# Kernel tuning notes

Measured on AMD Instinct MI355X. Metric: run time of the kernel, lower is better.

## Reference

```python
import jax, jax.numpy as jnp
import numpy as np

K = 3  # neighbors per sampled point (SetFeatureAbstraction k=3)


def fps_single(points, n_samples):
    """Farthest point sampling over one frame. points: [N, D]. Returns [n_samples] int32 idxs.
    Faithful to the torch loop: start at index 0, maintain min-distance-to-selected,
    pick argmax among remaining (selected points are masked to -inf)."""
    n = points.shape[0]

    def step(carry, _):
        dist, last = carry
        d = jnp.sum((points - points[last]) ** 2, axis=-1)   # squared dist to last added
        dist = jnp.minimum(dist, d)
        sel = jnp.argmax(dist).astype(jnp.int32)
        dist = dist.at[sel].set(-jnp.inf)                    # exclude from remaining
        return (dist, sel), sel

    dist0 = jnp.full((n,), jnp.inf, points.dtype).at[0].set(-jnp.inf)
    _, idxs = jax.lax.scan(step, (dist0, jnp.int32(0)), None, length=n_samples - 1)
    return jnp.concatenate([jnp.zeros((1,), jnp.int32), idxs])


def setup_inputs() -> dict:
    key = jax.random.key(0)
    ks = jax.random.split(key, 20)
    B, N, F, A, SD = 4, 8192, 64, 64, 5
    scale = lambda fan_in: 1.0 / np.sqrt(fan_in)
    def lin(k1, k2, out_d, in_d):
        s = scale(in_d)
        return (jax.random.uniform(k1, (out_d, in_d), jnp.float32, -s, s),
                jax.random.uniform(k2, (out_d,), jnp.float32, -s, s))
    w_in, b_in = lin(ks[0], ks[1], A, F)
    w_q, b_q = lin(ks[2], ks[3], A, A)
    w_k, b_k = lin(ks[4], ks[5], A, A)
    w_v, b_v = lin(ks[6], ks[7], A, A)
    w_h1, b_h1 = lin(ks[8], ks[9], A, A)
    w_h2, b_h2 = lin(ks[10], ks[11], A, A)
    w_out, b_out = lin(ks[12], ks[13], F, A)
    x = jax.random.normal(ks[14], (B, N, F), jnp.float32)
    spatial = jax.random.normal(ks[15], (B, N, SD), jnp.float32)
    return {"x": x, "spatial": spatial,
            "w_in": w_in, "b_in": b_in, "w_q": w_q, "b_q": b_q,
            "w_k": w_k, "b_k": b_k, "w_v": w_v, "b_v": b_v,
            "w_h1": w_h1, "b_h1": b_h1, "w_h2": w_h2, "b_h2": b_h2,
            "w_out": w_out, "b_out": b_out}


def reference(x, spatial, w_in, b_in, w_q, b_q, w_k, b_k, w_v, b_v,
              w_h1, b_h1, w_h2, b_h2, w_out, b_out):
    B, N, F = x.shape
    S = N // 2
    # ---- farthest point sampling (vmapped over batch) ----
    sample_idxs = jax.vmap(lambda p: fps_single(p, S))(spatial)          # [B, S]
    xs = jnp.take_along_axis(x, sample_idxs[..., None], axis=1)          # [B, S, F]
    sp = jnp.take_along_axis(spatial, sample_idxs[..., None], axis=1)    # [B, S, 5]
    # ---- kNN grouping: each sampled point gathers K nearest neighbors from full cloud ----
    d = jnp.sum((sp[:, :, None, :] - spatial[:, None, :, :]) ** 2, -1)   # [B, S, N]
    bidx = jnp.arange(B)[:, None]
    sidx = jnp.arange(S)[None, :]
    d = d.at[bidx, sidx, sample_idxs].set(jnp.inf)                        # exclude self
    _, knn_idx = jax.lax.top_k(-d, K)                                     # [B, S, K] smallest dists
    neigh_feat = jax.vmap(lambda xf, idx: xf[idx])(x, knn_idx)            # [B, S, K, F]
    # ---- subtract-based vector attention on sampled features ----
    t = xs @ w_in.T + b_in                                                # [B, S, A]
    q = t @ w_q.T + b_q
    k = t @ w_k.T + b_k
    v = t @ w_v.T + b_v
    h = jax.nn.relu((q - k) @ w_h1.T + b_h1) @ w_h2.T + b_h2
    w = jax.nn.softmax(h, axis=-1)                                        # per-channel weights
    out = (w * v) @ w_out.T + b_out + xs                                  # residual
    return out, neigh_feat
```

## Files before the change

kernel.cpp:

```cpp
#include <hip/hip_runtime.h>
#include <hip/hip_bf16.h>

#define NPTS 8192
#define SDIM 5
#define NBATCH 4
#define NS 4096
#define FEAT 64
#define KNN 3

#define WS_SIDX_OFF   0
#define WS_KNN_OFF    65536
#define WS_WT_OFF     262144

typedef float v2f __attribute__((ext_vector_type(2)));


__device__ __forceinline__ float sqdist5(float p0, float p1, float p2, float p3, float p4,
                                         float q0, float q1, float q2, float q3, float q4)
{
#pragma clang fp contract(off)
    float d0 = p0 - q0, d1 = p1 - q1, d2 = p2 - q2, d3 = p3 - q3, d4 = p4 - q4;
    float a = d0 * d0 + d1 * d1;
    a = a + d2 * d2;
    a = a + d3 * d3;
    a = a + d4 * d4;
    return a;
}

__device__ __forceinline__ float wave_max_f32_bcast(float v)
{
    int x;
    x = __builtin_amdgcn_update_dpp(0xFF800000, __float_as_int(v), 0x111, 0xf, 0xf, false);
    v = fmaxf(v, __int_as_float(x));
    x = __builtin_amdgcn_update_dpp(0xFF800000, __float_as_int(v), 0x112, 0xf, 0xf, false);
    v = fmaxf(v, __int_as_float(x));
    x = __builtin_amdgcn_update_dpp(0xFF800000, __float_as_int(v), 0x114, 0xf, 0xf, false);
    v = fmaxf(v, __int_as_float(x));
    x = __builtin_amdgcn_update_dpp(0xFF800000, __float_as_int(v), 0x118, 0xf, 0xf, false);
    v = fmaxf(v, __int_as_float(x));
    x = __builtin_amdgcn_update_dpp(0xFF800000, __float_as_int(v), 0x142, 0xf, 0xf, false);
    v = fmaxf(v, __int_as_float(x));
    x = __builtin_amdgcn_update_dpp(0xFF800000, __float_as_int(v), 0x143, 0xf, 0xf, false);
    v = fmaxf(v, __int_as_float(x));
    return __int_as_float(__builtin_amdgcn_readlane(__float_as_int(v), 63));
}

__device__ __forceinline__ int wave_min_i32_bcast(int v)
{
    int x;
    x = __builtin_amdgcn_update_dpp(0x7FFFFFFF, v, 0x111, 0xf, 0xf, false);
    v = min(v, x);
    x = __builtin_amdgcn_update_dpp(0x7FFFFFFF, v, 0x112, 0xf, 0xf, false);
    v = min(v, x);
    x = __builtin_amdgcn_update_dpp(0x7FFFFFFF, v, 0x114, 0xf, 0xf, false);
    v = min(v, x);
    x = __builtin_amdgcn_update_dpp(0x7FFFFFFF, v, 0x118, 0xf, 0xf, false);
    v = min(v, x);
    x = __builtin_amdgcn_update_dpp(0x7FFFFFFF, v, 0x142, 0xf, 0xf, false);
    v = min(v, x);
    x = __builtin_amdgcn_update_dpp(0x7FFFFFFF, v, 0x143, 0xf, 0xf, false);
    v = min(v, x);
    return __builtin_amdgcn_readlane(v, 63);
}

#define FOR_PAIRS(M) M(0) M(1) M(2) M(3) M(4) M(5) M(6) M(7)

__global__ __launch_bounds__(512, 2)
void fps_kernel(const float* __restrict__ spatial, int* __restrict__ sidx)
{
#pragma clang fp contract(off)
    const int b = blockIdx.x;
    const int t = threadIdx.x;
    const int lane = t & 63;
    const float* pts = spatial + (size_t)b * NPTS * SDIM;
    const float NEG_INF = -__builtin_inff();

#define DECL_PAIR(J) v2f px0_##J, px1_##J, px2_##J, px3_##J, px4_##J, dd_##J;
    FOR_PAIRS(DECL_PAIR)

#define LOAD_PAIR(J)                                                          \
    {                                                                         \
        const int ilo = (2 * J) * 512 + t;                                    \
        const int ihi = (2 * J + 1) * 512 + t;                                \
        px0_##J = (v2f){pts[ilo * SDIM + 0], pts[ihi * SDIM + 0]};            \
        px1_##J = (v2f){pts[ilo * SDIM + 1], pts[ihi * SDIM + 1]};            \
        px2_##J = (v2f){pts[ilo * SDIM + 2], pts[ihi * SDIM + 2]};            \
        px3_##J = (v2f){pts[ilo * SDIM + 3], pts[ihi * SDIM + 3]};            \
        px4_##J = (v2f){pts[ilo * SDIM + 4], pts[ihi * SDIM + 4]};            \
        dd_##J  = (v2f){__builtin_inff(), __builtin_inff()};                  \
    }
    FOR_PAIRS(LOAD_PAIR)

    if (t == 0) {
        dd_0.x = NEG_INF;
        sidx[b * NS] = 0;
    }

    __shared__ unsigned long long slot[4];
    if (t == 0) { slot[0] = 0; slot[1] = 0; slot[2] = 0; slot[3] = 0; }
    __syncthreads();

    int bsel = 0;
    for (int step = 1; step < NS; ++step) {
        const int p = step & 3;
        if (t == 0) slot[(step + 2) & 3] = 0;

        const float* qp = pts + bsel * SDIM;
        const float q0 = qp[0], q1 = qp[1], q2 = qp[2], q3 = qp[3], q4 = qp[4];
        const v2f q0v = {q0, q0}, q1v = {q1, q1}, q2v = {q2, q2},
                  q3v = {q3, q3}, q4v = {q4, q4};

        float bestv = NEG_INF;
        int   besti = 0;

#define UPD_PAIR(J)                                                           \
    {                                                                         \
        v2f t0 = px0_##J - q0v;                                               \
        v2f t1 = px1_##J - q1v;                                               \
        v2f t2 = px2_##J - q2v;                                               \
        v2f t3 = px3_##J - q3v;                                               \
        v2f t4 = px4_##J - q4v;                                               \
        v2f a = t0 * t0 + t1 * t1;      \
        a = a + t2 * t2;                                                      \
        a = a + t3 * t3;                                                      \
        a = a + t4 * t4;                                                      \
        v2f nd;                                                               \
        nd.x = fminf(dd_##J.x, a.x);                                          \
        nd.y = fminf(dd_##J.y, a.y);                                          \
        dd_##J = nd;                                                          \
        if (nd.x > bestv) { bestv = nd.x; besti = (2 * J) * 512 + t; }        \
        if (nd.y > bestv) { bestv = nd.y; besti = (2 * J + 1) * 512 + t; }    \
    }
        FOR_PAIRS(UPD_PAIR)

        const float maxv = wave_max_f32_bcast(bestv);
        const int   cand = (bestv == maxv) ? besti : 0x7FFFFFFF;
        const int   mini = wave_min_i32_bcast(cand);

        if (lane == 0) {
            const unsigned int kv = (maxv < 0.0f) ? 0u
                                                  : (__float_as_uint(maxv) | 0x80000000u);
            const unsigned long long key =
                ((unsigned long long)kv << 32) |
                (unsigned long long)(0xFFFFFFFFu - (unsigned)mini);
            atomicMax(&slot[p], key);
        }
        __syncthreads();

        const unsigned long long kk = slot[p];
        const int sel = (int)(0xFFFFFFFFu - (unsigned int)(kk & 0xFFFFFFFFull));
        bsel = __builtin_amdgcn_readfirstlane(sel);
        if (t == 0) sidx[b * NS + step] = sel;

        const int  jj  = bsel >> 9;
        const bool own = (bsel & 511) == t;

#define ZAP_PAIR(J)                                                           \
    {                                                                         \
        if (own && jj == 2 * J)     dd_##J.x = NEG_INF;                       \
        if (own && jj == 2 * J + 1) dd_##J.y = NEG_INF;                       \
    }
        FOR_PAIRS(ZAP_PAIR)
    }
}

__global__ __launch_bounds__(256)
void knn_kernel(const float* __restrict__ spatial, const int* __restrict__ sidx,
                int* __restrict__ knn)
{
    const int t   = threadIdx.x;
    const int sl  = t >> 3;
    const int r   = t & 7;
    const int spb = NS / 32;
    const int b   = blockIdx.x / spb;
    const int s   = (blockIdx.x % spb) * 32 + sl;
    const int self = sidx[b * NS + s];
    const float* pts = spatial + (size_t)b * NPTS * SDIM;

    const float q0 = pts[self * SDIM + 0], q1 = pts[self * SDIM + 1],
                q2 = pts[self * SDIM + 2], q3 = pts[self * SDIM + 3],
                q4 = pts[self * SDIM + 4];

    unsigned long long k0 = ~0ull, k1 = ~0ull, k2 = ~0ull;
    for (int i = r; i < NPTS; i += 8) {
        float a = sqdist5(pts[i * SDIM + 0], pts[i * SDIM + 1], pts[i * SDIM + 2],
                          pts[i * SDIM + 3], pts[i * SDIM + 4],
                          q0, q1, q2, q3, q4);
        unsigned long long key = ((unsigned long long)__float_as_uint(a) << 32) |
                                 (unsigned long long)(unsigned)i;
        if (i == self) key = ~0ull;
        if (key < k2) {
            if (key < k1) {
                k2 = k1;
                if (key < k0) { k1 = k0; k0 = key; } else k1 = key;
            } else k2 = key;
        }
    }

    __shared__ unsigned long long sk[256][3];
    sk[t][0] = k0; sk[t][1] = k1; sk[t][2] = k2;
    __syncthreads();

    if (r == 0) {
        unsigned long long b0 = ~0ull, b1 = ~0ull, b2 = ~0ull;
        for (int rr = 0; rr < 8; ++rr) {
#pragma unroll
            for (int m = 0; m < 3; ++m) {
                unsigned long long key = sk[(sl << 3) | rr][m];
                if (key < b2) {
                    if (key < b1) {
                        b2 = b1;
                        if (key < b0) { b1 = b0; b0 = key; } else b1 = key;
                    } else b2 = key;
                }
            }
        }
        const int basei = (b * NS + s) * KNN;
        knn[basei + 0] = (int)(b0 & 0xFFFFFFFFull);
        knn[basei + 1] = (int)(b1 & 0xFFFFFFFFull);
        knn[basei + 2] = (int)(b2 & 0xFFFFFFFFull);
    }
}

__global__ __launch_bounds__(256)
void gather_kernel(const float* __restrict__ x, const int* __restrict__ knn,
                   float* __restrict__ out2)
{
    const long long tid = (long long)blockIdx.x * 256 + threadIdx.x;
    const int       f   = (int)(tid & 63);
    const long long row = tid >> 6;
    const int       idx = knn[row];
    const int       b   = (int)(row / (NS * KNN));
    out2[tid] = x[((size_t)b * NPTS + idx) * FEAT + f];
}

__global__ __launch_bounds__(256)
void transpose_w(const float* __restrict__ w0, const float* __restrict__ w1,
                 const float* __restrict__ w2, const float* __restrict__ w3,
                 const float* __restrict__ w4, const float* __restrict__ w5,
                 const float* __restrict__ w6, float* __restrict__ wt)
{
    const float* w;
    switch (blockIdx.x) {
        case 0: w = w0; break; case 1: w = w1; break; case 2: w = w2; break;
        case 3: w = w3; break; case 4: w = w4; break; case 5: w = w5; break;
        default: w = w6; break;
    }
    float* o = wt + blockIdx.x * 4096;
    for (int e = threadIdx.x; e < 4096; e += 256) {
        const int r = e >> 6, c = e & 63;
        o[c * 64 + r] = w[e];
    }
}

__global__ __launch_bounds__(256)
void attn_kernel(const float* __restrict__ x, const int* __restrict__ sidx,
                 const float* __restrict__ wt,
                 const float* __restrict__ b_in, const float* __restrict__ b_q,
                 const float* __restrict__ b_k, const float* __restrict__ b_v,
                 const float* __restrict__ b_h1, const float* __restrict__ b_h2,
                 const float* __restrict__ b_out,
                 float* __restrict__ out)
{
    const int lane = threadIdx.x & 63;
    const int wid  = (int)((blockIdx.x * 256 + threadIdx.x) >> 6);
    const int b    = wid >> 12;
    const int si   = sidx[wid];
    const float xs = x[((size_t)b * NPTS + si) * FEAT + lane];

    const float* wt_in  = wt;
    const float* wt_q   = wt + 4096;
    const float* wt_k   = wt + 2 * 4096;
    const float* wt_v   = wt + 3 * 4096;
    const float* wt_h1  = wt + 4 * 4096;
    const float* wt_h2  = wt + 5 * 4096;
    const float* wt_out = wt + 6 * 4096;

    float tv = b_in[lane];
#pragma unroll
    for (int i = 0; i < 64; ++i) tv = fmaf(wt_in[i * 64 + lane], __shfl(xs, i), tv);

    float q = b_q[lane], k = b_k[lane], v = b_v[lane];
#pragma unroll
    for (int i = 0; i < 64; ++i) {
        const float ti = __shfl(tv, i);
        q = fmaf(wt_q[i * 64 + lane], ti, q);
        k = fmaf(wt_k[i * 64 + lane], ti, k);
        v = fmaf(wt_v[i * 64 + lane], ti, v);
    }
    const float d = q - k;
    float h = b_h1[lane];
#pragma unroll
    for (int i = 0; i < 64; ++i) h = fmaf(wt_h1[i * 64 + lane], __shfl(d, i), h);
    h = fmaxf(h, 0.0f);
    float h2 = b_h2[lane];
#pragma unroll
    for (int i = 0; i < 64; ++i) h2 = fmaf(wt_h2[i * 64 + lane], __shfl(h, i), h2);

    float m = h2;
#pragma unroll
    for (int off = 32; off > 0; off >>= 1) m = fmaxf(m, __shfl_xor(m, off));
    const float e = expf(h2 - m);
    float sum = e;
#pragma unroll
    for (int off = 32; off > 0; off >>= 1) sum += __shfl_xor(sum, off);
    const float u = (e / sum) * v;

    float o = b_out[lane];
#pragma unroll
    for (int i = 0; i < 64; ++i) o = fmaf(wt_out[i * 64 + lane], __shfl(u, i), o);
    o += xs;

    out[(size_t)wid * FEAT + lane] = o;
}

extern "C" void kernel_launch(void* const* d_in, const int* in_sizes, int n_in,
                              void* d_out, int out_size, void* d_ws, size_t ws_size,
                              hipStream_t stream)
{
    const float* x       = (const float*)d_in[0];
    const float* spatial = (const float*)d_in[1];
    const float* w_in    = (const float*)d_in[2];
    const float* b_in    = (const float*)d_in[3];
    const float* w_q     = (const float*)d_in[4];
    const float* b_q     = (const float*)d_in[5];
    const float* w_k     = (const float*)d_in[6];
    const float* b_k     = (const float*)d_in[7];
    const float* w_v     = (const float*)d_in[8];
    const float* b_v     = (const float*)d_in[9];
    const float* w_h1    = (const float*)d_in[10];
    const float* b_h1    = (const float*)d_in[11];
    const float* w_h2    = (const float*)d_in[12];
    const float* b_h2    = (const float*)d_in[13];
    const float* w_out   = (const float*)d_in[14];
    const float* b_out   = (const float*)d_in[15];

    int*   sidx = (int*)((char*)d_ws + WS_SIDX_OFF);
    int*   knn  = (int*)((char*)d_ws + WS_KNN_OFF);
    float* wt   = (float*)((char*)d_ws + WS_WT_OFF);

    float* out  = (float*)d_out;
    float* out2 = out + (size_t)NBATCH * NS * FEAT;

    hipLaunchKernelGGL(fps_kernel, dim3(NBATCH), dim3(512), 0, stream,
                       spatial, sidx);
    hipLaunchKernelGGL(transpose_w, dim3(7), dim3(256), 0, stream,
                       w_in, w_q, w_k, w_v, w_h1, w_h2, w_out, wt);
    hipLaunchKernelGGL(knn_kernel, dim3(NBATCH * NS / 32), dim3(256), 0, stream,
                       spatial, sidx, knn);
    hipLaunchKernelGGL(gather_kernel, dim3(NBATCH * NS * KNN * FEAT / 256), dim3(256),
                       0, stream, x, knn, out2);
    hipLaunchKernelGGL(attn_kernel, dim3(NBATCH * NS * FEAT / 256), dim3(256),
                       0, stream, x, sidx, wt,
                       b_in, b_q, b_k, b_v, b_h1, b_h2, b_out, out);
}
```

Before: 5.333 ms.

## Replace FPS block barrier and atomic with tagged per-wave LDS slots

```diff
diff --git a/kernel.cpp b/kernel.cpp
--- a/kernel.cpp
+++ b/kernel.cpp
@@ -72,6 +72,7 @@
     const int b = blockIdx.x;
     const int t = threadIdx.x;
     const int lane = t & 63;
+    const int wv = t >> 6;
     const float* pts = spatial + (size_t)b * NPTS * SDIM;
     const float NEG_INF = -__builtin_inff();
 
@@ -96,19 +97,19 @@
         sidx[b * NS] = 0;
     }
 
-    __shared__ unsigned long long slot[4];
-    if (t == 0) { slot[0] = 0; slot[1] = 0; slot[2] = 0; slot[3] = 0; }
+    volatile __shared__ unsigned long long ks[4][8];
+    volatile __shared__ float cc[4][8][5];
+    if (t < 32) ks[t >> 3][t & 7] = 0ull;
     __syncthreads();
 
-    int bsel = 0;
+    float qc0 = pts[0], qc1 = pts[1], qc2 = pts[2], qc3 = pts[3], qc4 = pts[4];
+
     for (int step = 1; step < NS; ++step) {
         const int p = step & 3;
-        if (t == 0) slot[(step + 2) & 3] = 0;
-
-        const float* qp = pts + bsel * SDIM;
-        const float q0 = qp[0], q1 = qp[1], q2 = qp[2], q3 = qp[3], q4 = qp[4];
-        const v2f q0v = {q0, q0}, q1v = {q1, q1}, q2v = {q2, q2},
-                  q3v = {q3, q3}, q4v = {q4, q4};
+        const unsigned int mytag = 0x80u | (unsigned)(step & 0x7F);
+
+        const v2f q0v = {qc0, qc0}, q1v = {qc1, qc1}, q2v = {qc2, qc2},
+                  q3v = {qc3, qc3}, q4v = {qc4, qc4};
 
         float bestv = NEG_INF;
         int   besti = 0;
@@ -137,30 +138,64 @@
         const int   cand = (bestv == maxv) ? besti : 0x7FFFFFFF;
         const int   mini = wave_min_i32_bcast(cand);
 
-        if (lane == 0) {
+        if (lane == (mini & 63)) {
+            volatile float* c = &cc[p][wv][0];
+            switch (mini >> 9) {
+#define PUB_CASE(J)                                                           \
+                case 2 * J:                                                   \
+                    c[0] = px0_##J.x; c[1] = px1_##J.x; c[2] = px2_##J.x;     \
+                    c[3] = px3_##J.x; c[4] = px4_##J.x; break;                \
+                case 2 * J + 1:                                               \
+                    c[0] = px0_##J.y; c[1] = px1_##J.y; c[2] = px2_##J.y;     \
+                    c[3] = px3_##J.y; c[4] = px4_##J.y; break;
+                FOR_PAIRS(PUB_CASE)
+            }
+            asm volatile("s_waitcnt lgkmcnt(0)" ::: "memory");
             const unsigned int kv = (maxv < 0.0f) ? 0u
                                                   : (__float_as_uint(maxv) | 0x80000000u);
-            const unsigned long long key =
-                ((unsigned long long)kv << 32) |
-                (unsigned long long)(0xFFFFFFFFu - (unsigned)mini);
-            atomicMax(&slot[p], key);
-        }
-        __syncthreads();
-
-        const unsigned long long kk = slot[p];
-        const int sel = (int)(0xFFFFFFFFu - (unsigned int)(kk & 0xFFFFFFFFull));
-        bsel = __builtin_amdgcn_readfirstlane(sel);
+            ks[p][wv] = ((unsigned long long)kv << 32) |
+                        ((unsigned long long)(0xFFFFu - (unsigned)mini) << 16) |
+                        (unsigned long long)mytag;
+        }
+
+        unsigned long long k0, k1, k2, k3, k4, k5, k6, k7;
+        for (;;) {
+            k0 = ks[p][0]; k1 = ks[p][1]; k2 = ks[p][2]; k3 = ks[p][3];
+            k4 = ks[p][4]; k5 = ks[p][5]; k6 = ks[p][6]; k7 = ks[p][7];
+            const unsigned int v0 = ((unsigned int)k0 ^ mytag) & 0xFFu;
+            const unsigned int v1 = ((unsigned int)k1 ^ mytag) & 0xFFu;
+            const unsigned int v2 = ((unsigned int)k2 ^ mytag) & 0xFFu;
+            const unsigned int v3 = ((unsigned int)k3 ^ mytag) & 0xFFu;
+            const unsigned int v4 = ((unsigned int)k4 ^ mytag) & 0xFFu;
+            const unsigned int v5 = ((unsigned int)k5 ^ mytag) & 0xFFu;
+            const unsigned int v6 = ((unsigned int)k6 ^ mytag) & 0xFFu;
+            const unsigned int v7 = ((unsigned int)k7 ^ mytag) & 0xFFu;
+            if ((v0 | v1 | v2 | v3 | v4 | v5 | v6 | v7) == 0u) break;
+        }
+        unsigned long long kk = k0;
+        if (k1 > kk) kk = k1;
+        if (k2 > kk) kk = k2;
+        if (k3 > kk) kk = k3;
+        if (k4 > kk) kk = k4;
+        if (k5 > kk) kk = k5;
+        if (k6 > kk) kk = k6;
+        if (k7 > kk) kk = k7;
+
+        const int sel = 0xFFFF - (int)((kk >> 16) & 0xFFFFull);
         if (t == 0) sidx[b * NS + step] = sel;
 
-        const int  jj  = bsel >> 9;
-        const bool own = (bsel & 511) == t;
-
-#define ZAP_PAIR(J)                                                           \
-    {                                                                         \
-        if (own && jj == 2 * J)     dd_##J.x = NEG_INF;                       \
-        if (own && jj == 2 * J + 1) dd_##J.y = NEG_INF;                       \
-    }
-        FOR_PAIRS(ZAP_PAIR)
+        const int selt = sel & 511;
+        if (selt == t) {
+            switch (sel >> 9) {
+#define ZAP_CASE(J)                                                           \
+                case 2 * J:     dd_##J.x = NEG_INF; break;                    \
+                case 2 * J + 1: dd_##J.y = NEG_INF; break;
+                FOR_PAIRS(ZAP_CASE)
+            }
+        }
+
+        volatile float* wc = &cc[p][selt >> 6][0];
+        qc0 = wc[0]; qc1 = wc[1]; qc2 = wc[2]; qc3 = wc[3]; qc4 = wc[4];
     }
 }
 
```

New measurement: 7.962 ms. +49.3%, slower.
